# Optimization experiments

Hardware: AMD Instinct MI355X
Metric: run time of the kernel (lower is better)

Reference implementation:

```python
import jax, jax.numpy as jnp
import numpy as np

B, T, C, J = 2048, 128, 3, 25   # batch, frames, coords, joints
E = 64                          # structure elements (n_elements)


def setup_inputs() -> dict:
    key = jax.random.key(0)
    k1, k2 = jax.random.split(key)
    x = jax.random.normal(k1, (B, T, C, J), dtype=jnp.float32)
    centres = jax.random.uniform(k2, (E, 2), dtype=jnp.float32)
    sharpness = jnp.full((E, 2), 3.0, dtype=jnp.float32)  # torch init: ones*3
    return {"x": x, "centres": centres, "sharpness": sharpness}


def _mst_deaths(Dm):
    """Prim's MST over dense distance matrix Dm [n,n].
    The multiset of MST edge weights equals the finite death times of the
    0-dim Vietoris-Rips persistence diagram (births are all 0)."""
    n = Dm.shape[0]
    in_tree0 = jnp.zeros(n, dtype=bool).at[0].set(True)

    def step(carry, _):
        mind, in_tree = carry
        masked = jnp.where(in_tree, jnp.inf, mind)  # distance from tree to each node
        j = jnp.argmin(masked)
        w = masked[j]                               # weight of edge added to MST
        in_tree = in_tree.at[j].set(True)
        mind = jnp.minimum(mind, Dm[j])
        return (mind, in_tree), w

    (_, _), deaths = jax.lax.scan(step, (Dm[0], in_tree0), None, length=n - 1)
    return deaths  # [n-1]


def reference(x, centres, sharpness):
    # --- dense preprocessing ---
    h = x.mean(1)                           # [B, C, J]
    h = h[..., :, None] - h[..., None, :]   # [B, C, J, J] pairwise coord diffs
    h = h.mean(-3)                          # [B, J, J]
    h = jnp.sqrt((h * h).sum(axis=1))       # torch.norm(., 2, dim=1) -> [B, J]
    lo, hi = h.min(), h.max()
    rng = hi - lo
    safe = rng > 1e-8
    h = jnp.where(safe, (h - lo) / jnp.where(safe, rng, 1.0), jnp.zeros_like(h))

    # --- Vietoris-Rips dim-0 persistence on point cloud h: B points in J dims ---
    sq = (h * h).sum(-1)
    d2 = sq[:, None] + sq[None, :] - 2.0 * (h @ h.T)       # [B, B]
    Dm = jnp.sqrt(jnp.maximum(d2, 1e-12))
    deaths = _mst_deaths(Dm)                               # [B-1]
    pd = jnp.stack([jnp.zeros_like(deaths), deaths], -1)[None]  # [1, P, 2]

    # --- StructureElementLayer: out[b,e] = sum_p exp(-sum_d s[e,d]^2 (pd-c)^2) ---
    s2 = sharpness * sharpness                             # [E, 2]
    diff = pd[:, :, None, :] - centres[None, None, :, :]   # [1, P, E, 2]
    out = jnp.exp(-(diff * diff * s2).sum(-1)).sum(1)      # [1, E]
    return out
```

## Files before the change

kernel.cpp:

```cpp
#include <hip/hip_runtime.h>
#include <math.h>

#define B_N 2048
#define T_N 128
#define C_N 3
#define J_N 25
#define E_N 64
#define TC  (T_N*C_N)
#define TCJ (TC*J_N)
#define NQ4 (TCJ/4)

#define D_OFF      0
#define H_OFF      (B_N*B_N)
#define BLO_OFF    (H_OFF + B_N*J_N)
#define BHI_OFF    (BLO_OFF + B_N)
#define DEATHS_OFF (BHI_OFF + B_N)
#define BEST_OFF   (DEATHS_OFF + B_N)
#define COMP_OFF   (BEST_OFF + 4*B_N)
#define GC_OFF     (COMP_OFF + 2*B_N)

typedef unsigned long long u64;
#define U64MAX 0xFFFFFFFFFFFFFFFFull

__global__ void __launch_bounds__(256) k_reduce(const float* __restrict__ x,
                                                float* __restrict__ ws) {
    __shared__ float4 part[250];
    __shared__ float S[100];
    __shared__ float Mj[25];
    const int t = threadIdx.x, b = blockIdx.x;
    const float4* x4 = (const float4*)(x + (size_t)b * TCJ);
    if (t < 250) {
        float4 a; a.x = a.y = a.z = a.w = 0.f;
        for (int idx = t; idx < NQ4; idx += 250) {
            float4 v = x4[idx];
            a.x += v.x; a.y += v.y; a.z += v.z; a.w += v.w;
        }
        part[t] = a;
    }
    __syncthreads();
    if (t < 25) {
        float4 s = part[t];
        #pragma unroll
        for (int g = 1; g < 10; ++g) {
            float4 v = part[t + 25 * g];
            s.x += v.x; s.y += v.y; s.z += v.z; s.w += v.w;
        }
        S[4*t] = s.x; S[4*t+1] = s.y; S[4*t+2] = s.z; S[4*t+3] = s.w;
    }
    __syncthreads();
    if (t < 25) Mj[t] = (S[t] + S[t+25] + S[t+50] + S[t+75]) * (1.0f / 384.0f);
    __syncthreads();
    if (t < 25) {
        float mj = Mj[t], acc = 0.f;
        #pragma unroll
        for (int i = 0; i < J_N; ++i) { float d = Mj[i] - mj; acc += d * d; }
        float hv = sqrtf(acc);
        ws[H_OFF + b * J_N + t] = hv;
        S[t] = hv;
    }
    __syncthreads();
    if (t == 0) {
        float lo = S[0], hi = S[0];
        #pragma unroll
        for (int i = 1; i < J_N; ++i) { lo = fminf(lo, S[i]); hi = fmaxf(hi, S[i]); }
        ws[BLO_OFF + b] = lo;
        ws[BHI_OFF + b] = hi;
    }
}

__global__ void k_dist(float* ws) {
    __shared__ float A[16][26], Bsh[16][26];
    const int tx = threadIdx.x, ty = threadIdx.y;
    const int flat = ty * 16 + tx;
    const int rowA = blockIdx.x * 16, rowB = blockIdx.y * 16;
    const float* h = ws + H_OFF;
    for (int idx = flat; idx < 16 * J_N; idx += 256) {
        int r = idx / J_N, c = idx % J_N;
        A[r][c]   = h[(rowA + r) * J_N + c];
        Bsh[r][c] = h[(rowB + r) * J_N + c];
    }
    __syncthreads();
    float acc = 0.f;
    #pragma unroll
    for (int k = 0; k < J_N; ++k) {
        float d = A[ty][k] - Bsh[tx][k];
        acc += d * d;
    }
    float* D = ws + D_OFF;
    D[(size_t)(rowA + ty) * B_N + rowB + tx] = sqrtf(fmaxf(acc, 1e-12f));
}

__global__ void __launch_bounds__(1024) k_scan0(float* __restrict__ ws) {
    const int t = threadIdx.x, w = t >> 6, lane = t & 63;
    const int row = blockIdx.x * 16 + w;
    const float4* row4 = (const float4*)(ws + D_OFF + (size_t)row * B_N);
    u64 best = U64MAX;
    #pragma unroll
    for (int k = 0; k < 8; ++k) {
        const int q = k * 64 + lane;
        float4 w4 = row4[q];
        const unsigned j0 = (unsigned)(q * 4);
        float wv[4] = {w4.x, w4.y, w4.z, w4.w};
        #pragma unroll
        for (int m = 0; m < 4; ++m) {
            unsigned j = j0 + m;
            if (j != (unsigned)row) {
                unsigned a = min((unsigned)row, j), b2 = max((unsigned)row, j);
                u64 key = ((u64)__float_as_uint(wv[m]) << 32) | (a << 11) | b2;
                if (key < best) best = key;
            }
        }
    }
    #pragma unroll
    for (int off = 32; off; off >>= 1) {
        u64 o = __shfl_down(best, off);
        if (o < best) best = o;
    }
    if (lane == 0) ((u64*)(ws + BEST_OFF))[row] = best;
    if (blockIdx.x == 0) {
        unsigned* gc = (unsigned*)(ws + COMP_OFF);
        gc[t] = (unsigned)t; gc[t + 1024] = (unsigned)(t + 1024);
        if (t == 0) { ((unsigned*)(ws + GC_OFF))[0] = 0u; ((unsigned*)(ws + GC_OFF))[1] = 0u; }
    }
}

__global__ void __launch_bounds__(1024) k_round(float* __restrict__ ws, int par_in) {
    unsigned* gcnt = (unsigned*)(ws + GC_OFF);
    const unsigned base = gcnt[par_in];
    if (base >= B_N - 1) return;
    __shared__ __align__(16) unsigned comp[B_N];
    __shared__ u64 cb[B_N];
    __shared__ unsigned par[B_N];
    __shared__ unsigned cnt_s;
    const int t = threadIdx.x, blk = blockIdx.x;
    const unsigned* gcomp_in = (const unsigned*)(ws + COMP_OFF) + par_in * B_N;
    unsigned* gcomp_out = (unsigned*)(ws + COMP_OFF) + (par_in ^ 1) * B_N;
    const u64* bin = (const u64*)(ws + BEST_OFF) + par_in * B_N;
    u64* bout = (u64*)(ws + BEST_OFF) + (par_in ^ 1) * B_N;
    float* deaths = ws + DEATHS_OFF;

    if (t == 0) cnt_s = 0u;
    comp[t] = gcomp_in[t]; comp[t + 1024] = gcomp_in[t + 1024];
    cb[t] = U64MAX; cb[t + 1024] = U64MAX;
    __syncthreads();
    #pragma unroll
    for (int i = t; i < B_N; i += 1024) {
        u64 bk = bin[i];
        if (bk != U64MAX) atomicMin(&cb[comp[i]], bk);
    }
    __syncthreads();
    #pragma unroll
    for (int c = t; c < B_N; c += 1024) {
        u64 k = cb[c];
        unsigned p = (unsigned)c;
        if (k != U64MAX) {
            unsigned a  = (unsigned)((k >> 11) & 0x7FFu);
            unsigned b2 = (unsigned)(k & 0x7FFu);
            unsigned ca = comp[a], cbv = comp[b2];
            unsigned c2 = (ca == (unsigned)c) ? cbv : ca;
            p = c2;
            if (!(cb[c2] == k && c2 < (unsigned)c)) {
                unsigned li = atomicAdd(&cnt_s, 1u);
                if (blk == 0) deaths[base + li] = __uint_as_float((unsigned)(k >> 32));
            }
        }
        par[c] = p;
    }
    __syncthreads();
    #pragma unroll
    for (int c = t; c < B_N; c += 1024) {
        unsigned p = par[c];
        if (p != (unsigned)c && par[p] == (unsigned)c && (unsigned)c < p) par[c] = (unsigned)c;
    }
    __syncthreads();
    #pragma unroll
    for (int c = t; c < B_N; c += 1024) {
        unsigned r = par[c];
        while (true) { unsigned pr = par[r]; if (pr == r) break; r = pr; }
        par[c] = r;
    }
    __syncthreads();
    #pragma unroll
    for (int i = t; i < B_N; i += 1024) comp[i] = par[comp[i]];
    __syncthreads();
    const unsigned newbase = base + cnt_s;
    const bool conv = (newbase >= B_N - 1);
    if (blk == 0) {
        gcomp_out[t] = comp[t]; gcomp_out[t + 1024] = comp[t + 1024];
        if (t == 0) { gcnt[par_in ^ 1] = newbase; if (conv) gcnt[par_in] = newbase; }
    }
    if (conv) return;

    const int w = t >> 6, lane = t & 63;
    const int row = blk * 16 + w;
    const unsigned ci = comp[row];
    const float4* row4 = (const float4*)(ws + D_OFF + (size_t)row * B_N);
    const uint4* comp4 = (const uint4*)comp;
    u64 best = U64MAX;
    #pragma unroll
    for (int k = 0; k < 8; ++k) {
        const int q = k * 64 + lane;
        float4 w4 = row4[q];
        uint4  c4 = comp4[q];
        const unsigned j0 = (unsigned)(q * 4);
        float wv[4] = {w4.x, w4.y, w4.z, w4.w};
        unsigned cv[4] = {c4.x, c4.y, c4.z, c4.w};
        #pragma unroll
        for (int m = 0; m < 4; ++m) {
            if (cv[m] != ci) {
                unsigned j = j0 + m;
                unsigned a = min((unsigned)row, j), b2 = max((unsigned)row, j);
                u64 key = ((u64)__float_as_uint(wv[m]) << 32) | (a << 11) | b2;
                if (key < best) best = key;
            }
        }
    }
    #pragma unroll
    for (int off = 32; off; off >>= 1) {
        u64 o = __shfl_down(best, off);
        if (o < best) best = o;
    }
    if (lane == 0) bout[row] = best;
}

__global__ void __launch_bounds__(1024) k_final(float* __restrict__ ws,
                                                const float* __restrict__ centres,
                                                const float* __restrict__ sharp,
                                                float* __restrict__ out) {
    __shared__ __align__(16) unsigned comp[B_N];
    __shared__ u64 cb[B_N];
    __shared__ unsigned par[B_N];
    __shared__ unsigned cnt_s;
    __shared__ float redlo[16], redhi[16];
    const int t = threadIdx.x;
    unsigned* gcnt = (unsigned*)(ws + GC_OFF);
    float* deaths = ws + DEATHS_OFF;
    const unsigned base = gcnt[0];
    if (base < B_N - 1) {
        const unsigned* gcomp_in = (const unsigned*)(ws + COMP_OFF);
        const u64* bin = (const u64*)(ws + BEST_OFF);
        if (t == 0) cnt_s = 0u;
        comp[t] = gcomp_in[t]; comp[t + 1024] = gcomp_in[t + 1024];
        cb[t] = U64MAX; cb[t + 1024] = U64MAX;
        __syncthreads();
        #pragma unroll
        for (int i = t; i < B_N; i += 1024) {
            u64 bk = bin[i];
            if (bk != U64MAX) atomicMin(&cb[comp[i]], bk);
        }
        __syncthreads();
        #pragma unroll
        for (int c = t; c < B_N; c += 1024) {
            u64 k = cb[c];
            if (k != U64MAX) {
                unsigned a  = (unsigned)((k >> 11) & 0x7FFu);
                unsigned b2 = (unsigned)(k & 0x7FFu);
                unsigned ca = comp[a], cbv = comp[b2];
                unsigned c2 = (ca == (unsigned)c) ? cbv : ca;
                if (!(cb[c2] == k && c2 < (unsigned)c)) {
                    unsigned li = atomicAdd(&cnt_s, 1u);
                    deaths[base + li] = __uint_as_float((unsigned)(k >> 32));
                }
            }
        }
        __syncthreads();
    }
    const int w = t >> 6, lane = t & 63;
    float lo = INFINITY, hi = -INFINITY;
    #pragma unroll
    for (int i = t; i < B_N; i += 1024) {
        lo = fminf(lo, ws[BLO_OFF + i]);
        hi = fmaxf(hi, ws[BHI_OFF + i]);
    }
    #pragma unroll
    for (int off = 32; off; off >>= 1) {
        lo = fminf(lo, __shfl_down(lo, off));
        hi = fmaxf(hi, __shfl_down(hi, off));
    }
    if (lane == 0) { redlo[w] = lo; redhi[w] = hi; }
    __syncthreads();
    lo = redlo[0]; hi = redhi[0];
    #pragma unroll
    for (int k = 1; k < 16; ++k) { lo = fminf(lo, redlo[k]); hi = fmaxf(hi, redhi[k]); }
    float rng = hi - lo;
    float rinv = (rng > 1e-8f) ? 1.0f / rng : 0.0f;

    for (int e = w; e < E_N; e += 16) {
        const float c0 = centres[e * 2], c1 = centres[e * 2 + 1];
        const float s0 = sharp[e * 2],   s1 = sharp[e * 2 + 1];
        const float s1sq = s1 * s1;
        float acc = 0.f;
        for (int p = lane; p < B_N - 1; p += 64) {
            float d = deaths[p] * rinv - c1;
            acc += expf(-s1sq * d * d);
        }
        #pragma unroll
        for (int off = 32; off; off >>= 1) acc += __shfl_down(acc, off);
        if (lane == 0) out[e] = expf(-s0 * s0 * c0 * c0) * acc;
    }
}

extern "C" void kernel_launch(void* const* d_in, const int* in_sizes, int n_in,
                              void* d_out, int out_size, void* d_ws, size_t ws_size,
                              hipStream_t stream) {
    const float* x       = (const float*)d_in[0];
    const float* centres = (const float*)d_in[1];
    const float* sharp   = (const float*)d_in[2];
    float* out = (float*)d_out;
    float* ws  = (float*)d_ws;

    hipLaunchKernelGGL(k_reduce, dim3(B_N),      dim3(256),    0, stream, x, ws);
    hipLaunchKernelGGL(k_dist,   dim3(128, 128), dim3(16, 16), 0, stream, ws);
    hipLaunchKernelGGL(k_scan0,  dim3(128),      dim3(1024),   0, stream, ws);
    for (int r = 0; r < 10; ++r)
        hipLaunchKernelGGL(k_round, dim3(128), dim3(1024), 0, stream, ws, r & 1);
    hipLaunchKernelGGL(k_final, dim3(1), dim3(1024), 0, stream, ws, centres, sharp, out);
}
```

Baseline: 191.6 us.

## Contract Boruvka components into 64x64 graph and finish MST in one block

Replaces the fixed ten Boruvka rounds with four full scan rounds plus one merge-only round. The surviving components (assumed at most 64) are then contracted into a 64x64 inter-component min-edge matrix using shared atomics, and a single block finishes the MST on that small graph. Rows whose previous best edge still crosses components reuse that edge instead of rescanning the distance row. The goal is to cut repeated full B×B distance scans and kernel launches. The risk is that more than 64 components remain after four rounds, which would overflow the contraction table.

Measured after the change: 187.3 us. 2.2% less time.

```diff
diff --git a/kernel.cpp b/kernel.cpp
--- a/kernel.cpp
+++ b/kernel.cpp
@@ -18,9 +18,11 @@
 #define BEST_OFF   (DEATHS_OFF + B_N)
 #define COMP_OFF   (BEST_OFF + 4*B_N)
 #define GC_OFF     (COMP_OFF + 2*B_N)
+#define DC_OFF     (GC_OFF + 2)
 
 typedef unsigned long long u64;
 #define U64MAX 0xFFFFFFFFFFFFFFFFull
+#define U32INF 0xFFFFFFFFu
 
 __global__ void __launch_bounds__(256) k_reduce(const float* __restrict__ x,
                                                 float* __restrict__ ws) {
@@ -120,11 +122,15 @@
     if (blockIdx.x == 0) {
         unsigned* gc = (unsigned*)(ws + COMP_OFF);
         gc[t] = (unsigned)t; gc[t + 1024] = (unsigned)(t + 1024);
+        unsigned* dc = (unsigned*)(ws + DC_OFF);
+        #pragma unroll
+        for (int i = 0; i < 4; ++i) dc[i * 1024 + t] = U32INF;
         if (t == 0) { ((unsigned*)(ws + GC_OFF))[0] = 0u; ((unsigned*)(ws + GC_OFF))[1] = 0u; }
     }
 }
 
-__global__ void __launch_bounds__(1024) k_round(float* __restrict__ ws, int par_in) {
+__global__ void __launch_bounds__(1024) k_round(float* __restrict__ ws, int par_in,
+                                                int do_scan) {
     unsigned* gcnt = (unsigned*)(ws + GC_OFF);
     const unsigned base = gcnt[par_in];
     if (base >= B_N - 1) return;
@@ -184,16 +190,25 @@
     for (int i = t; i < B_N; i += 1024) comp[i] = par[comp[i]];
     __syncthreads();
     const unsigned newbase = base + cnt_s;
-    const bool conv = (newbase >= B_N - 1);
     if (blk == 0) {
         gcomp_out[t] = comp[t]; gcomp_out[t + 1024] = comp[t + 1024];
-        if (t == 0) { gcnt[par_in ^ 1] = newbase; if (conv) gcnt[par_in] = newbase; }
-    }
-    if (conv) return;
+        if (t == 0) { gcnt[par_in ^ 1] = newbase; if (newbase >= B_N - 1) gcnt[par_in] = newbase; }
+    }
+    if (!do_scan || newbase >= B_N - 1) return;
 
     const int w = t >> 6, lane = t & 63;
     const int row = blk * 16 + w;
     const unsigned ci = comp[row];
+    u64 prev = bin[row];
+    {
+        unsigned pa = (unsigned)((prev >> 11) & 0x7FFu);
+        unsigned pb = (unsigned)(prev & 0x7FFu);
+        unsigned jo = (pa == (unsigned)row) ? pb : pa;
+        if (comp[jo] != ci) {
+            if (lane == 0) bout[row] = prev;
+            return;
+        }
+    }
     const float4* row4 = (const float4*)(ws + D_OFF + (size_t)row * B_N);
     const uint4* comp4 = (const uint4*)comp;
     u64 best = U64MAX;
@@ -223,49 +238,156 @@
     if (lane == 0) bout[row] = best;
 }
 
-__global__ void __launch_bounds__(1024) k_final(float* __restrict__ ws,
-                                                const float* __restrict__ centres,
-                                                const float* __restrict__ sharp,
-                                                float* __restrict__ out) {
-    __shared__ __align__(16) unsigned comp[B_N];
-    __shared__ u64 cb[B_N];
-    __shared__ unsigned par[B_N];
-    __shared__ unsigned cnt_s;
+__global__ void __launch_bounds__(1024) k_contract(float* __restrict__ ws) {
+    if (((const unsigned*)(ws + GC_OFF))[1] >= B_N - 1) return;
+    __shared__ unsigned cflag[B_N];
+    __shared__ unsigned Dcs[64 * 64];
+    __shared__ unsigned csum[16];
+    const int t = threadIdx.x, blk = blockIdx.x;
+    const unsigned lane = t & 63, w = t >> 6;
+    const unsigned* gcomp1 = (const unsigned*)(ws + COMP_OFF) + B_N;
+
+    cflag[t] = 0u; cflag[t + 1024] = 0u;
+    #pragma unroll
+    for (int i = 0; i < 4; ++i) Dcs[i * 1024 + t] = U32INF;
+    __syncthreads();
+    unsigned cA = gcomp1[t], cB = gcomp1[t + 1024];
+    cflag[cA] = 1u; cflag[cB] = 1u;
+    __syncthreads();
+    unsigned f0 = cflag[2 * t], f1 = cflag[2 * t + 1];
+    unsigned s = f0 + f1, sc = s;
+    #pragma unroll
+    for (int off = 1; off < 64; off <<= 1) {
+        unsigned v = __shfl_up(sc, off);
+        if (lane >= (unsigned)off) sc += v;
+    }
+    if (lane == 63) csum[w] = sc;
+    __syncthreads();
+    if (t < 16) {
+        unsigned v = csum[t], acc = v;
+        #pragma unroll
+        for (int off = 1; off < 16; off <<= 1) {
+            unsigned u2 = __shfl_up(acc, off);
+            if (t >= off) acc += u2;
+        }
+        csum[t] = acc - v;
+    }
+    __syncthreads();
+    unsigned off0 = csum[w] + (sc - s);
+    __syncthreads();
+    if (f0) cflag[2 * t] = off0;
+    if (f1) cflag[2 * t + 1] = off0 + f0;
+    __syncthreads();
+
+    #pragma unroll
+    for (int q2 = 0; q2 < 2; ++q2) {
+        const int row = blk * 32 + (int)w * 2 + q2;
+        const unsigned ci = gcomp1[row];
+        const unsigned ri = cflag[ci];
+        const float4* row4 = (const float4*)(ws + D_OFF + (size_t)row * B_N);
+        const uint4* comp4 = (const uint4*)gcomp1;
+        #pragma unroll
+        for (int k = 0; k < 8; ++k) {
+            const int q = k * 64 + (int)lane;
+            float4 w4 = row4[q];
+            uint4  c4 = comp4[q];
+            float wv[4] = {w4.x, w4.y, w4.z, w4.w};
+            unsigned cv[4] = {c4.x, c4.y, c4.z, c4.w};
+            #pragma unroll
+            for (int m = 0; m < 4; ++m) {
+                if (cv[m] != ci) {
+                    unsigned rj = cflag[cv[m]];
+                    atomicMin(&Dcs[ri * 64 + rj], __float_as_uint(wv[m]));
+                }
+            }
+        }
+    }
+    __syncthreads();
+    unsigned* gDc = (unsigned*)(ws + DC_OFF);
+    #pragma unroll
+    for (int i = t; i < 4096; i += 1024) {
+        unsigned v = Dcs[i];
+        if (v != U32INF) atomicMin(&gDc[i], v);
+    }
+}
+
+__global__ void __launch_bounds__(1024) k_finishstruct(float* __restrict__ ws,
+                                                       const float* __restrict__ centres,
+                                                       const float* __restrict__ sharp,
+                                                       float* __restrict__ out) {
+    __shared__ unsigned Dcs[64 * 64];
+    __shared__ u64 cbf[64];
+    __shared__ unsigned parf[64], ccomp[64];
+    __shared__ unsigned cnt_s, base_s;
     __shared__ float redlo[16], redhi[16];
     const int t = threadIdx.x;
-    unsigned* gcnt = (unsigned*)(ws + GC_OFF);
+    const unsigned lane = t & 63, w = t >> 6;
     float* deaths = ws + DEATHS_OFF;
-    const unsigned base = gcnt[0];
-    if (base < B_N - 1) {
-        const unsigned* gcomp_in = (const unsigned*)(ws + COMP_OFF);
-        const u64* bin = (const u64*)(ws + BEST_OFF);
-        if (t == 0) cnt_s = 0u;
-        comp[t] = gcomp_in[t]; comp[t + 1024] = gcomp_in[t + 1024];
-        cb[t] = U64MAX; cb[t + 1024] = U64MAX;
+    const unsigned base0 = ((const unsigned*)(ws + GC_OFF))[1];
+
+    if (base0 < B_N - 1) {
+        const unsigned* gDc = (const unsigned*)(ws + DC_OFF);
+        #pragma unroll
+        for (int i = 0; i < 4; ++i) Dcs[i * 1024 + t] = gDc[i * 1024 + t];
+        if (t < 64) ccomp[t] = (unsigned)t;
+        if (t == 0) base_s = base0;
         __syncthreads();
-        #pragma unroll
-        for (int i = t; i < B_N; i += 1024) {
-            u64 bk = bin[i];
-            if (bk != U64MAX) atomicMin(&cb[comp[i]], bk);
-        }
+        for (int iter = 0; iter < 7; ++iter) {
+            if (t < 64) cbf[t] = U64MAX;
+            if (t == 0) cnt_s = 0u;
+            __syncthreads();
+            #pragma unroll
+            for (int q2 = 0; q2 < 4; ++q2) {
+                const int r = (int)w * 4 + q2;
+                const unsigned cc = ccomp[r];
+                unsigned wv = Dcs[r * 64 + lane];
+                u64 key = U64MAX;
+                if (wv != U32INF && ccomp[lane] != cc) {
+                    unsigned a = min((unsigned)r, lane), b2 = max((unsigned)r, lane);
+                    key = ((u64)wv << 32) | (a << 6) | b2;
+                }
+                #pragma unroll
+                for (int off = 32; off; off >>= 1) {
+                    u64 o = __shfl_down(key, off);
+                    if (o < key) key = o;
+                }
+                if (lane == 0 && key != U64MAX) atomicMin(&cbf[cc], key);
+            }
+            __syncthreads();
+            if (w == 0) {
+                u64 k = cbf[lane];
+                unsigned p = lane;
+                bool add = false; float dw = 0.f;
+                if (k != U64MAX) {
+                    unsigned a = (unsigned)((k >> 6) & 63u), b2 = (unsigned)(k & 63u);
+                    unsigned ca = ccomp[a], cbv = ccomp[b2];
+                    unsigned c2 = (ca == lane) ? cbv : ca;
+                    p = c2;
+                    if (!(cbf[c2] == k && c2 < lane)) {
+                        add = true; dw = __uint_as_float((unsigned)(k >> 32));
+                    }
+                }
+                parf[lane] = p;
+                unsigned pp = parf[lane];
+                if (pp != lane && parf[pp] == lane && lane < pp) parf[lane] = lane;
+                unsigned r2 = parf[lane];
+                while (parf[r2] != r2) r2 = parf[r2];
+                parf[lane] = r2;
+                if (add) {
+                    unsigned li = atomicAdd(&cnt_s, 1u);
+                    deaths[base_s + li] = dw;
+                }
+                ccomp[lane] = parf[ccomp[lane]];
+            }
+            __syncthreads();
+            if (t == 0) base_s += cnt_s;
+            __syncthreads();
+            if (base_s >= B_N - 1) break;
+        }
+        __threadfence_block();
         __syncthreads();
-        #pragma unroll
-        for (int c = t; c < B_N; c += 1024) {
-            u64 k = cb[c];
-            if (k != U64MAX) {
-                unsigned a  = (unsigned)((k >> 11) & 0x7FFu);
-                unsigned b2 = (unsigned)(k & 0x7FFu);
-                unsigned ca = comp[a], cbv = comp[b2];
-                unsigned c2 = (ca == (unsigned)c) ? cbv : ca;
-                if (!(cb[c2] == k && c2 < (unsigned)c)) {
-                    unsigned li = atomicAdd(&cnt_s, 1u);
-                    deaths[base + li] = __uint_as_float((unsigned)(k >> 32));
-                }
-            }
-        }
-        __syncthreads();
-    }
-    const int w = t >> 6, lane = t & 63;
+    }
+
     float lo = INFINITY, hi = -INFINITY;
     #pragma unroll
     for (int i = t; i < B_N; i += 1024) {
@@ -285,12 +407,12 @@
     float rng = hi - lo;
     float rinv = (rng > 1e-8f) ? 1.0f / rng : 0.0f;
 
-    for (int e = w; e < E_N; e += 16) {
+    for (int e = (int)w; e < E_N; e += 16) {
         const float c0 = centres[e * 2], c1 = centres[e * 2 + 1];
         const float s0 = sharp[e * 2],   s1 = sharp[e * 2 + 1];
         const float s1sq = s1 * s1;
         float acc = 0.f;
-        for (int p = lane; p < B_N - 1; p += 64) {
+        for (int p = (int)lane; p < B_N - 1; p += 64) {
             float d = deaths[p] * rinv - c1;
             acc += expf(-s1sq * d * d);
         }
@@ -309,10 +431,14 @@
     float* out = (float*)d_out;
     float* ws  = (float*)d_ws;
 
-    hipLaunchKernelGGL(k_reduce, dim3(B_N),      dim3(256),    0, stream, x, ws);
-    hipLaunchKernelGGL(k_dist,   dim3(128, 128), dim3(16, 16), 0, stream, ws);
-    hipLaunchKernelGGL(k_scan0,  dim3(128),      dim3(1024),   0, stream, ws);
-    for (int r = 0; r < 10; ++r)
-        hipLaunchKernelGGL(k_round, dim3(128), dim3(1024), 0, stream, ws, r & 1);
-    hipLaunchKernelGGL(k_final, dim3(1), dim3(1024), 0, stream, ws, centres, sharp, out);
-}
+    hipLaunchKernelGGL(k_reduce,   dim3(B_N),      dim3(256),    0, stream, x, ws);
+    hipLaunchKernelGGL(k_dist,     dim3(128, 128), dim3(16, 16), 0, stream, ws);
+    hipLaunchKernelGGL(k_scan0,    dim3(128),      dim3(1024),   0, stream, ws);
+    hipLaunchKernelGGL(k_round,    dim3(128),      dim3(1024),   0, stream, ws, 0, 1);
+    hipLaunchKernelGGL(k_round,    dim3(128),      dim3(1024),   0, stream, ws, 1, 1);
+    hipLaunchKernelGGL(k_round,    dim3(128),      dim3(1024),   0, stream, ws, 0, 1);
+    hipLaunchKernelGGL(k_round,    dim3(128),      dim3(1024),   0, stream, ws, 1, 1);
+    hipLaunchKernelGGL(k_round,    dim3(128),      dim3(1024),   0, stream, ws, 0, 0);
+    hipLaunchKernelGGL(k_contract, dim3(64),       dim3(1024),   0, stream, ws);
+    hipLaunchKernelGGL(k_finishstruct, dim3(1),    dim3(1024),   0, stream, ws, centres, sharp, out);
+}
```
